# Optimization experiments

Measured on AMD Instinct MI355X. Metric: run time of the kernel, lower is better.

Reference implementation:

```python
import jax, jax.numpy as jnp
import numpy as np

N, E, IN, H, OUT, G = 50000, 600000, 128, 128, 10, 64


def gcn_conv(x, src, dst, W, b, n):
    # PyG GCNConv: x' = D^{-1/2} (A + I) D^{-1/2} (x W) + b
    h = x @ W
    ones = jnp.ones(src.shape[0], x.dtype)
    deg = jax.ops.segment_sum(ones, dst, num_segments=n) + 1.0  # +1 for self-loop
    dinv = jax.lax.rsqrt(deg)
    norm = dinv[src] * dinv[dst]                                 # [E]
    agg = jax.ops.segment_sum(h[src] * norm[:, None], dst, num_segments=n)
    agg = agg + h * (1.0 / deg)[:, None]                         # self-loop term
    return agg + b


def setup_inputs() -> dict:
    key = jax.random.key(0)
    ks = jax.random.split(key, 12)
    s = 1.0 / np.sqrt(H)
    return {
        "x": jax.random.normal(ks[0], (N, IN), jnp.float32),
        "edge_index": jax.random.randint(ks[1], (2, E), 0, N, dtype=jnp.int32),
        "batch": jnp.sort(jax.random.randint(ks[2], (N,), 0, G, dtype=jnp.int32)),
        "W1": jax.random.normal(ks[3], (IN, H), jnp.float32) * s,
        "b1": jnp.zeros((H,), jnp.float32),
        "W2": jax.random.normal(ks[4], (H, H), jnp.float32) * s,
        "b2": jnp.zeros((H,), jnp.float32),
        "W3": jax.random.normal(ks[5], (H, H), jnp.float32) * s,
        "b3": jnp.zeros((H,), jnp.float32),
        "Wfc": jax.random.normal(ks[6], (H, OUT), jnp.float32) * s,
        "bfc": jnp.zeros((OUT,), jnp.float32),
    }


def reference(x, edge_index, batch, W1, b1, W2, b2, W3, b3, Wfc, bfc):
    src, dst = edge_index[0], edge_index[1]
    h = jax.nn.relu(gcn_conv(x, src, dst, W1, b1, N))
    h = jax.nn.relu(gcn_conv(h, src, dst, W2, b2, N))
    h = jax.nn.relu(gcn_conv(h, src, dst, W3, b3, N))
    # global mean pool over graphs
    sums = jax.ops.segment_sum(h, batch, num_segments=G)
    cnt = jax.ops.segment_sum(jnp.ones(N, h.dtype), batch, num_segments=G)
    pooled = sums / jnp.maximum(cnt, 1.0)[:, None]               # [G, H]
    return pooled @ Wfc + bfc                                    # [G, OUT]
```

## Files before the change

### kernel.cpp

```cpp
#include <hip/hip_runtime.h>


#define N_NODES 50000
#define N_EDGES 600000
#define DIM 128
#define OUT_DIM 10
#define N_GRAPHS 64
#define STRIP 128
#define GR 64
#define SCAN_G ((N_NODES + 255) / 256)

__global__ void zero_kernel(int* __restrict__ p, int n) {
    int i = blockIdx.x * blockDim.x + threadIdx.x;
    for (; i < n; i += gridDim.x * blockDim.x) p[i] = 0;
}

__global__ void hist_kernel(const int* __restrict__ dst, int* __restrict__ deg) {
    int e = blockIdx.x * blockDim.x + threadIdx.x;
    if (e < N_EDGES) atomicAdd(&deg[dst[e]], 1);
}

__global__ __launch_bounds__(256) void scan_local_kernel(const int* __restrict__ deg,
                                                         int* __restrict__ locx,
                                                         int* __restrict__ bsum,
                                                         float* __restrict__ dinv,
                                                         float* __restrict__ invdeg) {
    __shared__ int lds[256];
    int tid = threadIdx.x;
    int i = blockIdx.x * 256 + tid;
    int d = (i < N_NODES) ? deg[i] : 0;
    int v = d;
    lds[tid] = v;
    __syncthreads();
#pragma unroll
    for (int off = 1; off < 256; off <<= 1) {
        int t = (tid >= off) ? lds[tid - off] : 0;
        __syncthreads();
        v += t;
        lds[tid] = v;
        __syncthreads();
    }
    if (i < N_NODES) {
        locx[i] = v - d;
        float df = (float)d + 1.0f;
        dinv[i]   = rsqrtf(df);
        invdeg[i] = 1.0f / df;
    }
    if (tid == 255) bsum[blockIdx.x] = v;
}

__global__ __launch_bounds__(256) void scan_block_kernel(const int* __restrict__ bsum,
                                                         int* __restrict__ boff) {
    __shared__ int lds[256];
    int tid = threadIdx.x;
    int d = (tid < SCAN_G) ? bsum[tid] : 0;
    int v = d;
    lds[tid] = v;
    __syncthreads();
#pragma unroll
    for (int off = 1; off < 256; off <<= 1) {
        int t = (tid >= off) ? lds[tid - off] : 0;
        __syncthreads();
        v += t;
        lds[tid] = v;
        __syncthreads();
    }
    if (tid < SCAN_G) boff[tid] = v - d;
}

__global__ void scan_apply_kernel(const int* __restrict__ locx, const int* __restrict__ boff,
                                  int* __restrict__ startv) {
    int i = blockIdx.x * blockDim.x + threadIdx.x;
    if (i < N_NODES) startv[i] = locx[i] + boff[blockIdx.x];
}

__global__ void csr_build_kernel(const int* __restrict__ src, const int* __restrict__ dst,
                                 const int* __restrict__ start, int* __restrict__ cursor,
                                 const float* __restrict__ dinv,
                                 int2* __restrict__ csr_pair) {
    int e = blockIdx.x * blockDim.x + threadIdx.x;
    if (e < N_EDGES) {
        int s = src[e], d = dst[e];
        int slot = start[d] + atomicAdd(&cursor[d], 1);
        int2 rec;
        rec.x = s;
        rec.y = __float_as_int(dinv[s] * dinv[d]);
        csr_pair[slot] = rec;
    }
}

__global__ __launch_bounds__(256) void gemm_kernel(const float* __restrict__ A,
                                                   const float* __restrict__ W,
                                                   float* __restrict__ C) {
    __shared__ float4 Alds[GR][DIM / 4];
    int row0 = blockIdx.x * GR;
    int tid  = threadIdx.x;
    for (int i = tid; i < GR * (DIM / 4); i += 256) {
        int r = i >> 5, c = i & 31;
        int gr = row0 + r;
        Alds[r][c] = (gr < N_NODES) ? ((const float4*)A)[(size_t)gr * 32 + c]
                                    : make_float4(0.f, 0.f, 0.f, 0.f);
    }
    __syncthreads();
    int tx = tid & 31;
    int ty = tid >> 5;
    float acc[8][4];
#pragma unroll
    for (int r = 0; r < 8; ++r)
#pragma unroll
        for (int c = 0; c < 4; ++c) acc[r][c] = 0.f;
    const float4* W4 = (const float4*)W;
    for (int k = 0; k < DIM; k += 4) {
        float4 a[8];
#pragma unroll
        for (int r = 0; r < 8; ++r) a[r] = Alds[ty * 8 + r][k >> 2];
        float4 w0 = W4[(k + 0) * 32 + tx];
        float4 w1 = W4[(k + 1) * 32 + tx];
        float4 w2 = W4[(k + 2) * 32 + tx];
        float4 w3 = W4[(k + 3) * 32 + tx];
#pragma unroll
        for (int r = 0; r < 8; ++r) {
            acc[r][0] += a[r].x * w0.x + a[r].y * w1.x + a[r].z * w2.x + a[r].w * w3.x;
            acc[r][1] += a[r].x * w0.y + a[r].y * w1.y + a[r].z * w2.y + a[r].w * w3.y;
            acc[r][2] += a[r].x * w0.z + a[r].y * w1.z + a[r].z * w2.z + a[r].w * w3.z;
            acc[r][3] += a[r].x * w0.w + a[r].y * w1.w + a[r].z * w2.w + a[r].w * w3.w;
        }
    }
#pragma unroll
    for (int r = 0; r < 8; ++r) {
        int gr = row0 + ty * 8 + r;
        if (gr < N_NODES) {
            float4 o = make_float4(acc[r][0], acc[r][1], acc[r][2], acc[r][3]);
            ((float4*)C)[(size_t)gr * 32 + tx] = o;
        }
    }
}

__global__ __launch_bounds__(256) void pull_kernel(const float* __restrict__ HW,
                                                   const int2* __restrict__ csr_pair,
                                                   const int* __restrict__ start,
                                                   const int* __restrict__ deg,
                                                   const float* __restrict__ invdeg,
                                                   const float* __restrict__ bias,
                                                   float* __restrict__ Fout) {
    int wid  = threadIdx.x >> 6;
    int lane = threadIdx.x & 63;
    int half = blockIdx.x & 1;
    int node = (blockIdx.x >> 1) * 4 + wid;
    if (node >= N_NODES) return;
    int f = half * 64 + lane;
    int st = start[node];
    int dg = deg[node];
    float ax = 0.f;
    for (int base = 0; base < dg; base += 64) {
        int m = min(dg - base, 64);
        int2 rec = (lane < m) ? csr_pair[st + base + lane] : make_int2(0, 0);
        int   si = rec.x;
        float wi = __int_as_float(rec.y);
        int idx = 0;
        for (; idx + 8 <= m; idx += 8) {
            int s0 = __shfl(si, idx);     int s1 = __shfl(si, idx + 1);
            int s2 = __shfl(si, idx + 2); int s3 = __shfl(si, idx + 3);
            int s4 = __shfl(si, idx + 4); int s5 = __shfl(si, idx + 5);
            int s6 = __shfl(si, idx + 6); int s7 = __shfl(si, idx + 7);
            float w0 = __shfl(wi, idx);     float w1 = __shfl(wi, idx + 1);
            float w2 = __shfl(wi, idx + 2); float w3 = __shfl(wi, idx + 3);
            float w4 = __shfl(wi, idx + 4); float w5 = __shfl(wi, idx + 5);
            float w6 = __shfl(wi, idx + 6); float w7 = __shfl(wi, idx + 7);
            float v0 = HW[(size_t)s0 * DIM + f];
            float v1 = HW[(size_t)s1 * DIM + f];
            float v2 = HW[(size_t)s2 * DIM + f];
            float v3 = HW[(size_t)s3 * DIM + f];
            float v4 = HW[(size_t)s4 * DIM + f];
            float v5 = HW[(size_t)s5 * DIM + f];
            float v6 = HW[(size_t)s6 * DIM + f];
            float v7 = HW[(size_t)s7 * DIM + f];
            ax += v0 * w0 + v1 * w1 + v2 * w2 + v3 * w3
                + v4 * w4 + v5 * w5 + v6 * w6 + v7 * w7;
        }
        for (; idx < m; ++idx) {
            int s = __shfl(si, idx);
            float w = __shfl(wi, idx);
            ax += HW[(size_t)s * DIM + f] * w;
        }
    }
    ax += HW[(size_t)node * DIM + f] * invdeg[node];
    ax = fmaxf(ax + bias[f], 0.f);
    Fout[(size_t)node * DIM + f] = ax;
}

__global__ void bounds_kernel(const int* __restrict__ batch,
                              int* __restrict__ startg, int* __restrict__ endg) {
    int i = blockIdx.x * blockDim.x + threadIdx.x;
    if (i >= N_NODES) return;
    int b = batch[i];
    if (i == 0 || batch[i - 1] != b) startg[b] = i;
    if (i == N_NODES - 1 || batch[i + 1] != b) endg[b] = i + 1;
}

__global__ __launch_bounds__(128) void pool_kernel(const float* __restrict__ F,
                                                   const int* __restrict__ batch,
                                                   float* __restrict__ pooled) {
    int s0 = blockIdx.x * STRIP;
    int f  = threadIdx.x;
    if (s0 >= N_NODES) return;
    int end = min(s0 + STRIP, N_NODES);
    int cur = batch[s0];
    float acc = 0.f;
    for (int n = s0; n < end; ++n) {
        int bn = batch[n];
        if (bn != cur) {
            atomicAdd(&pooled[cur * DIM + f], acc);
            acc = 0.f; cur = bn;
        }
        acc += F[(size_t)n * DIM + f];
    }
    atomicAdd(&pooled[cur * DIM + f], acc);
}

__global__ __launch_bounds__(640) void fc_kernel(const float* __restrict__ pooled,
                                                 const int* __restrict__ startg,
                                                 const int* __restrict__ endg,
                                                 const float* __restrict__ Wfc,
                                                 const float* __restrict__ bfc,
                                                 float* __restrict__ out) {
    int t = threadIdx.x;
    if (t >= N_GRAPHS * OUT_DIM) return;
    int g = t / OUT_DIM, o = t % OUT_DIM;
    int c = endg[g] - startg[g];
    float inv = 1.0f / fmaxf((float)c, 1.0f);
    float acc = bfc[o];
#pragma unroll 8
    for (int k = 0; k < DIM; ++k)
        acc += pooled[g * DIM + k] * inv * Wfc[k * OUT_DIM + o];
    out[g * OUT_DIM + o] = acc;
}

extern "C" void kernel_launch(void* const* d_in, const int* in_sizes, int n_in,
                              void* d_out, int out_size, void* d_ws, size_t ws_size,
                              hipStream_t stream) {
    const float* x    = (const float*)d_in[0];
    const int*   ei   = (const int*)d_in[1];
    const int*   batch= (const int*)d_in[2];
    const float* W1   = (const float*)d_in[3];
    const float* b1   = (const float*)d_in[4];
    const float* W2   = (const float*)d_in[5];
    const float* b2   = (const float*)d_in[6];
    const float* W3   = (const float*)d_in[7];
    const float* b3   = (const float*)d_in[8];
    const float* Wfc  = (const float*)d_in[9];
    const float* bfc  = (const float*)d_in[10];
    float* out = (float*)d_out;

    const int* src = ei;
    const int* dst = ei + N_EDGES;

    char* ws = (char*)d_ws;
    size_t o = 0;
    float* HW   = (float*)(ws + o); o += (size_t)N_NODES * DIM * 4;
    float* PB   = (float*)(ws + o); o += (size_t)N_NODES * DIM * 4;
    int*   deg    = (int*)(ws + o); o += (size_t)N_NODES * 4;
    int*   cursor = (int*)(ws + o); o += (size_t)N_NODES * 4;
    float* pooled = (float*)(ws + o); o += (size_t)N_GRAPHS * DIM * 4;
    int*   startg = (int*)(ws + o); o += (size_t)N_GRAPHS * 4;
    int*   endg   = (int*)(ws + o); o += (size_t)N_GRAPHS * 4;
    int*   startv = (int*)(ws + o); o += (size_t)N_NODES * 4;
    float* dinv   = (float*)(ws + o); o += (size_t)N_NODES * 4;
    float* invdeg = (float*)(ws + o); o += (size_t)N_NODES * 4;
    int*   locx   = (int*)(ws + o); o += (size_t)N_NODES * 4;
    int*   bsum   = (int*)(ws + o); o += (size_t)SCAN_G * 4;
    int*   boff   = (int*)(ws + o); o += (size_t)SCAN_G * 4;
    o = (o + 7) & ~(size_t)7;
    int2*  csr_pair = (int2*)(ws + o); o += (size_t)N_EDGES * 8;

    const int nzero = 2 * N_NODES + N_GRAPHS * DIM + 2 * N_GRAPHS;

    zero_kernel<<<(nzero + 255) / 256, 256, 0, stream>>>(deg, nzero);
    hist_kernel<<<(N_EDGES + 255) / 256, 256, 0, stream>>>(dst, deg);
    scan_local_kernel<<<SCAN_G, 256, 0, stream>>>(deg, locx, bsum, dinv, invdeg);
    scan_block_kernel<<<1, 256, 0, stream>>>(bsum, boff);
    scan_apply_kernel<<<SCAN_G, 256, 0, stream>>>(locx, boff, startv);
    csr_build_kernel<<<(N_EDGES + 255) / 256, 256, 0, stream>>>(src, dst, startv, cursor,
                                                                dinv, csr_pair);

    const int ggrid = (N_NODES + GR - 1) / GR;
    const int pgrid = 2 * ((N_NODES + 3) / 4);

    gemm_kernel<<<ggrid, 256, 0, stream>>>(x, W1, HW);
    pull_kernel<<<pgrid, 256, 0, stream>>>(HW, csr_pair, startv, deg, invdeg, b1, PB);
    gemm_kernel<<<ggrid, 256, 0, stream>>>(PB, W2, HW);
    pull_kernel<<<pgrid, 256, 0, stream>>>(HW, csr_pair, startv, deg, invdeg, b2, PB);
    gemm_kernel<<<ggrid, 256, 0, stream>>>(PB, W3, HW);
    pull_kernel<<<pgrid, 256, 0, stream>>>(HW, csr_pair, startv, deg, invdeg, b3, PB);

    bounds_kernel<<<(N_NODES + 255) / 256, 256, 0, stream>>>(batch, startg, endg);
    pool_kernel<<<(N_NODES + STRIP - 1) / STRIP, 128, 0, stream>>>(PB, batch, pooled);
    fc_kernel<<<1, 640, 0, stream>>>(pooled, startg, endg, Wfc, bfc, out);
}
```

Measured before the change: 468.0 us.

## Vectorize pull aggregation with float4 loads and split edges across half-waves

The pull kernel now handles all 128 features of a node in one wavefront. Each half-wave loads a full 512-byte row as float4 and processes alternate edges, and the two halves are combined with a cross-lane shuffle reduction. Before, each row was split across two blocks, which loaded the CSR entries twice and issued scalar loads. This halves the CSR index traffic and the grid size and widens the memory requests, at the cost of an extra shuffle reduction and idle upper lanes during the final write.

```diff
diff --git a/kernel.cpp b/kernel.cpp
--- a/kernel.cpp
+++ b/kernel.cpp
@@ -145,48 +145,61 @@
                                                    float* __restrict__ Fout) {
     int wid  = threadIdx.x >> 6;
     int lane = threadIdx.x & 63;
-    int half = blockIdx.x & 1;
-    int node = (blockIdx.x >> 1) * 4 + wid;
+    int node = blockIdx.x * 4 + wid;
     if (node >= N_NODES) return;
-    int f = half * 64 + lane;
+    int hi = lane >> 5;
+    int l  = lane & 31;
+    const float4* HW4 = (const float4*)HW;
     int st = start[node];
     int dg = deg[node];
-    float ax = 0.f;
+    float  iv = invdeg[node];
+    float4 hs = HW4[(size_t)node * 32 + l];
+    float4 bb = ((const float4*)bias)[l];
+    float4 acc = make_float4(0.f, 0.f, 0.f, 0.f);
     for (int base = 0; base < dg; base += 64) {
         int m = min(dg - base, 64);
         int2 rec = (lane < m) ? csr_pair[st + base + lane] : make_int2(0, 0);
         int   si = rec.x;
         float wi = __int_as_float(rec.y);
-        int idx = 0;
-        for (; idx + 8 <= m; idx += 8) {
-            int s0 = __shfl(si, idx);     int s1 = __shfl(si, idx + 1);
-            int s2 = __shfl(si, idx + 2); int s3 = __shfl(si, idx + 3);
-            int s4 = __shfl(si, idx + 4); int s5 = __shfl(si, idx + 5);
-            int s6 = __shfl(si, idx + 6); int s7 = __shfl(si, idx + 7);
-            float w0 = __shfl(wi, idx);     float w1 = __shfl(wi, idx + 1);
-            float w2 = __shfl(wi, idx + 2); float w3 = __shfl(wi, idx + 3);
-            float w4 = __shfl(wi, idx + 4); float w5 = __shfl(wi, idx + 5);
-            float w6 = __shfl(wi, idx + 6); float w7 = __shfl(wi, idx + 7);
-            float v0 = HW[(size_t)s0 * DIM + f];
-            float v1 = HW[(size_t)s1 * DIM + f];
-            float v2 = HW[(size_t)s2 * DIM + f];
-            float v3 = HW[(size_t)s3 * DIM + f];
-            float v4 = HW[(size_t)s4 * DIM + f];
-            float v5 = HW[(size_t)s5 * DIM + f];
-            float v6 = HW[(size_t)s6 * DIM + f];
-            float v7 = HW[(size_t)s7 * DIM + f];
-            ax += v0 * w0 + v1 * w1 + v2 * w2 + v3 * w3
-                + v4 * w4 + v5 * w5 + v6 * w6 + v7 * w7;
-        }
-        for (; idx < m; ++idx) {
-            int s = __shfl(si, idx);
-            float w = __shfl(wi, idx);
-            ax += HW[(size_t)s * DIM + f] * w;
-        }
-    }
-    ax += HW[(size_t)node * DIM + f] * invdeg[node];
-    ax = fmaxf(ax + bias[f], 0.f);
-    Fout[(size_t)node * DIM + f] = ax;
+        int npair = (m + 1) >> 1;
+        int p = 0;
+        for (; p + 4 <= npair; p += 4) {
+            int i0 = 2 * (p + 0) + hi, i1 = 2 * (p + 1) + hi;
+            int i2 = 2 * (p + 2) + hi, i3 = 2 * (p + 3) + hi;
+            int s0 = __shfl(si, i0), s1 = __shfl(si, i1);
+            int s2 = __shfl(si, i2), s3 = __shfl(si, i3);
+            float w0 = __shfl(wi, i0), w1 = __shfl(wi, i1);
+            float w2 = __shfl(wi, i2), w3 = __shfl(wi, i3);
+            float4 v0 = HW4[(size_t)s0 * 32 + l];
+            float4 v1 = HW4[(size_t)s1 * 32 + l];
+            float4 v2 = HW4[(size_t)s2 * 32 + l];
+            float4 v3 = HW4[(size_t)s3 * 32 + l];
+            acc.x += v0.x * w0; acc.y += v0.y * w0; acc.z += v0.z * w0; acc.w += v0.w * w0;
+            acc.x += v1.x * w1; acc.y += v1.y * w1; acc.z += v1.z * w1; acc.w += v1.w * w1;
+            acc.x += v2.x * w2; acc.y += v2.y * w2; acc.z += v2.z * w2; acc.w += v2.w * w2;
+            acc.x += v3.x * w3; acc.y += v3.y * w3; acc.z += v3.z * w3; acc.w += v3.w * w3;
+        }
+        for (; p < npair; ++p) {
+            int i0 = 2 * p + hi;
+            int s0 = __shfl(si, i0);
+            float w0 = __shfl(wi, i0);
+            float4 v0 = HW4[(size_t)s0 * 32 + l];
+            acc.x += v0.x * w0; acc.y += v0.y * w0; acc.z += v0.z * w0; acc.w += v0.w * w0;
+        }
+    }
+    acc.x += __shfl(acc.x, lane + 32);
+    acc.y += __shfl(acc.y, lane + 32);
+    acc.z += __shfl(acc.z, lane + 32);
+    acc.w += __shfl(acc.w, lane + 32);
+    if (lane < 32) {
+        acc.x += hs.x * iv; acc.y += hs.y * iv;
+        acc.z += hs.z * iv; acc.w += hs.w * iv;
+        acc.x = fmaxf(acc.x + bb.x, 0.f);
+        acc.y = fmaxf(acc.y + bb.y, 0.f);
+        acc.z = fmaxf(acc.z + bb.z, 0.f);
+        acc.w = fmaxf(acc.w + bb.w, 0.f);
+        ((float4*)Fout)[(size_t)node * 32 + l] = acc;
+    }
 }
 
 __global__ void bounds_kernel(const int* __restrict__ batch,
@@ -284,7 +297,7 @@
                                                                 dinv, csr_pair);
 
     const int ggrid = (N_NODES + GR - 1) / GR;
-    const int pgrid = 2 * ((N_NODES + 3) / 4);
+    const int pgrid = (N_NODES + 3) / 4;
 
     gemm_kernel<<<ggrid, 256, 0, stream>>>(x, W1, HW);
     pull_kernel<<<pgrid, 256, 0, stream>>>(HW, csr_pair, startv, deg, invdeg, b1, PB);
```

After: 437.0 us. 1.07x faster.
